# Kernel optimization log

Measured on AMD Instinct MI355X. Metric: run time of the kernel, lower is better.

Reference implementation:

```python
import jax, jax.numpy as jnp
import numpy as np

B, N_TOK, D = 32, 1024, 1024
CH, PS, NP = 3, 16, 32  # channels, patch_size, n_patches (sample_size // patch_size)
EPS = 1e-5


def setup_inputs() -> dict:
    key = jax.random.key(0)
    k1, k2 = jax.random.split(key)
    x = jax.random.normal(k1, (B, N_TOK, D), dtype=jnp.float32)
    ln_w = jnp.ones((D,), dtype=jnp.float32)
    ln_b = jnp.zeros((D,), dtype=jnp.float32)
    W = jax.random.normal(k2, (CH * PS * PS, D), dtype=jnp.float32) * (1.0 / np.sqrt(D))
    b = jnp.zeros((CH * PS * PS,), dtype=jnp.float32)
    return {"x": x, "ln_w": ln_w, "ln_b": ln_b, "W": W, "b": b}


def reference(x, ln_w, ln_b, W, b):
    # LayerNorm over last dim
    mean = jnp.mean(x, axis=-1, keepdims=True)
    var = jnp.mean(jnp.square(x - mean), axis=-1, keepdims=True)
    h = (x - mean) * jax.lax.rsqrt(var + EPS) * ln_w + ln_b
    # SiLU
    h = h * jax.nn.sigmoid(h)
    # Linear: [B, N, D] @ [D, ph*pw*c] + bias
    y = jnp.einsum('bnd,od->bno', h, W) + b  # [B, N_TOK, PS*PS*CH]
    # rearrange 'b (h w) (ph pw c) -> b c (h ph) (w pw)'
    y = y.reshape(B, NP, NP, PS, PS, CH)           # b h w ph pw c
    y = y.transpose(0, 5, 1, 3, 2, 4)              # b c h ph w pw
    y = y.reshape(B, CH, NP * PS, NP * PS)
    return y
```

## Files before the change

kernel.cpp:

```cpp
#include <hip/hip_runtime.h>
#include <hip/hip_bf16.h>

#define M_TOT 32768
#define DDIM  1024
#define ODIM  768
#define LN_EPS 1e-5f

typedef __attribute__((__ext_vector_type__(8))) short bf16x8;
typedef __attribute__((__ext_vector_type__(4))) float f32x4;

__device__ __forceinline__ unsigned short f2bf(float f) {
  union { __hip_bfloat16 h; unsigned short u; } cv;
  cv.h = __float2bfloat16(f);
  return cv.u;
}

__device__ __forceinline__ float silu_f(float v) {
  return v / (1.f + __expf(-v));
}

__global__ void wconv_kernel(const float4* __restrict__ Wf, ushort4* __restrict__ Wb, int n4) {
  int i = blockIdx.x * blockDim.x + threadIdx.x;
  if (i >= n4) return;
  float4 v = Wf[i];
  ushort4 o;
  o.x = f2bf(v.x); o.y = f2bf(v.y); o.z = f2bf(v.z); o.w = f2bf(v.w);
  Wb[i] = o;
}

__global__ __launch_bounds__(256)
void ln_silu_kernel(const float* __restrict__ x, const float* __restrict__ lnw,
                    const float* __restrict__ lnb, __hip_bfloat16* __restrict__ h)
{
  const int tid  = threadIdx.x;
  const int lane = tid & 63;
  const int wid  = tid >> 6;
  const int row  = blockIdx.x * 4 + wid;

  const float4* xr = (const float4*)(x + (size_t)row * DDIM);
  float4 v[4];
#pragma unroll
  for (int jj = 0; jj < 4; ++jj) v[jj] = xr[lane + 64 * jj];

  float s = 0.f, ss = 0.f;
#pragma unroll
  for (int jj = 0; jj < 4; ++jj) {
    float4 a = v[jj];
    s  += a.x + a.y + a.z + a.w;
    ss += a.x * a.x + a.y * a.y + a.z * a.z + a.w * a.w;
  }
#pragma unroll
  for (int off = 1; off < 64; off <<= 1) {
    s  += __shfl_xor(s, off);
    ss += __shfl_xor(ss, off);
  }
  const float mean = s * (1.f / 1024.f);
  const float rstd = rsqrtf(ss * (1.f / 1024.f) - mean * mean + LN_EPS);

  ushort4* hr = (ushort4*)(h + (size_t)row * DDIM);
#pragma unroll
  for (int jj = 0; jj < 4; ++jj) {
    float4 wv = ((const float4*)lnw)[lane + 64 * jj];
    float4 bv = ((const float4*)lnb)[lane + 64 * jj];
    float4 a  = v[jj];
    float e0 = silu_f((a.x - mean) * rstd * wv.x + bv.x);
    float e1 = silu_f((a.y - mean) * rstd * wv.y + bv.y);
    float e2 = silu_f((a.z - mean) * rstd * wv.z + bv.z);
    float e3 = silu_f((a.w - mean) * rstd * wv.w + bv.w);
    ushort4 o; o.x = f2bf(e0); o.y = f2bf(e1); o.z = f2bf(e2); o.w = f2bf(e3);
    hr[lane + 64 * jj] = o;
  }
}

#define GBM 128
#define GBN 192
#define ABYTES 8192
#define BUFB   20480
#define GLDS   61440

__device__ __forceinline__ void gload16(const void* g, void* l) {
  __builtin_amdgcn_global_load_lds(
      (const __attribute__((address_space(1))) unsigned int*)g,
      (__attribute__((address_space(3))) unsigned int*)l, 16, 0, 0);
}

#define VMW(n) asm volatile("s_waitcnt vmcnt(" #n ")" ::: "memory")

__global__ __launch_bounds__(512, 4)
void gemm_kernel(const __hip_bfloat16* __restrict__ h,
                 const __hip_bfloat16* __restrict__ Wb,
                 const float* __restrict__ bias,
                 float* __restrict__ out)
{
  extern __shared__ char smem[];
  const int tid  = threadIdx.x;
  const int lane = tid & 63;
  const int w    = tid >> 6;

  const int wg = blockIdx.x;
  const int sv = ((wg & 7) << 7) + (wg >> 3);
  const int mt = sv >> 2, nt = sv & 3;
  const int m0 = mt * GBM, n0 = nt * GBN;

  const int aRow = tid >> 2;
  const int aSrc = ((tid & 3) ^ (aRow & 3)) << 3;
  const __hip_bfloat16* aPtr = h + (size_t)(m0 + aRow) * DDIM + aSrc;

  const int bRow0 = tid >> 2;
  const int bSrc0 = ((tid & 3) ^ (bRow0 & 3)) << 3;
  const __hip_bfloat16* bPtr0 = Wb + (size_t)(n0 + bRow0) * DDIM + bSrc0;
  const int s1    = 512 + tid;
  const int bRow1 = s1 >> 2;
  const int bSrc1 = ((s1 & 3) ^ (bRow1 & 3)) << 3;
  const __hip_bfloat16* bPtr1 = Wb + (size_t)(n0 + bRow1) * DDIM + bSrc1;
  const bool doB1 = (tid < 256);

  const int wm = w >> 2, wn = w & 3;
  const int lr = lane & 15, lq = lane >> 4;
  int aRd[4], bRd[3];
#pragma unroll
  for (int i = 0; i < 4; ++i) {
    int row = wm * 64 + i * 16 + lr;
    aRd[i] = row * 64 + ((lq ^ (row & 3)) << 4);
  }
#pragma unroll
  for (int j = 0; j < 3; ++j) {
    int row = wn * 48 + j * 16 + lr;
    bRd[j] = ABYTES + row * 64 + ((lq ^ (row & 3)) << 4);
  }

  auto stage = [&](int t) {
    const int k0  = t << 5;
    char* base = smem + (t % 3) * BUFB;
    gload16(aPtr + k0, base + (tid << 4));
    gload16(bPtr0 + k0, base + ABYTES + (tid << 4));
    if (doB1) gload16(bPtr1 + k0, base + ABYTES + (s1 << 4));
  };

  f32x4 acc[4][3];
#pragma unroll
  for (int i = 0; i < 4; ++i)
#pragma unroll
    for (int j = 0; j < 3; ++j)
      acc[i][j] = (f32x4){0.f, 0.f, 0.f, 0.f};

  stage(0); stage(1); stage(2);

  for (int t = 0; t < 32; ++t) {
    if (t <= 29)      { if (w < 4) VMW(6); else VMW(4); }
    else if (t == 30) { if (w < 4) VMW(3); else VMW(2); }
    else              { VMW(0); }
    __builtin_amdgcn_s_barrier();
    asm volatile("" ::: "memory");

    const char* bb = smem + (t % 3) * BUFB;
    bf16x8 af[4], bfq[3];
#pragma unroll
    for (int i = 0; i < 4; ++i) af[i] = *(const bf16x8*)(bb + aRd[i]);
#pragma unroll
    for (int j = 0; j < 3; ++j) bfq[j] = *(const bf16x8*)(bb + bRd[j]);

    __builtin_amdgcn_s_setprio(1);
#pragma unroll
    for (int i = 0; i < 4; ++i)
#pragma unroll
      for (int j = 0; j < 3; ++j)
        acc[i][j] = __builtin_amdgcn_mfma_f32_16x16x32_bf16(af[i], bfq[j], acc[i][j], 0, 0, 0);
    __builtin_amdgcn_s_setprio(0);

    asm volatile("s_waitcnt lgkmcnt(0)" ::: "memory");
    __builtin_amdgcn_s_barrier();
    asm volatile("" ::: "memory");
    if (t <= 28) stage(t + 3);
  }

  const int b   = m0 >> 10;
  const int hq0 = (m0 & 1023) >> 5;
  float bv[3]; int cj[3], pwj[3], prj[3];
#pragma unroll
  for (int j = 0; j < 3; ++j) {
    int o = wn * 48 + j * 16 + lr;
    bv[j]  = bias[n0 + o];
    cj[j]  = o % 3;
    int oq = o / 3;
    pwj[j] = oq & 15;
    prj[j] = o / 48;
  }
  float* ldsF = (float*)smem;

#pragma unroll
  for (int g = 0; g < 8; ++g) {
    if (wm == (g >> 2)) {
      const int i_f = g & 3;
#pragma unroll
      for (int j = 0; j < 3; ++j)
#pragma unroll
        for (int r = 0; r < 4; ++r) {
          const int tk = lq * 4 + r;
          ldsF[((cj[j] * 4 + prj[j]) << 8) + (tk << 4) + (pwj[j] ^ (lq << 2))] =
              acc[i_f][j][r] + bv[j];
        }
    }
    __syncthreads();
    const int hq = hq0 + (g >> 1);
#pragma unroll
    for (int q = 0; q < 2; ++q) {
      if (q == 1 && tid >= 256) break;
      const int f   = (q << 9) + tid;
      const int c   = f >> 8;
      const int pr  = (f >> 6) & 3;
      const int tk  = (f >> 2) & 15;
      const int pw0 = (f & 3) << 2;
      const int lqw = tk >> 2;
      float4 v = *(const float4*)(ldsF + (((c * 4 + pr) << 8) + (tk << 4) + (pw0 ^ (lqw << 2))));
      const size_t idx = (((size_t)(b * 3 + c)) << 18)
                       + (size_t)((hq << 4) + (nt << 2) + pr) * 512
                       + ((g & 1) << 8) + (tk << 4) + pw0;
      *(float4*)(out + idx) = v;
    }
    __syncthreads();
  }
}

#define BM 64
#define BK 32
#define NTHR 1024
#define LDS_BYTES 53760

__global__ __launch_bounds__(NTHR, 4)
void fused_kernel(const float* __restrict__ x,
                  const float* __restrict__ lnw,
                  const float* __restrict__ lnb,
                  const float* __restrict__ Wf,
                  const float* __restrict__ bias,
                  float* __restrict__ out)
{
  extern __shared__ char smem[];
  char* AsBase = smem;
  char* BsBase = smem + 4096;
  float* smean = (float*)(smem + 53248);
  float* srstd = smean + BM;

  const int tid = threadIdx.x;
  const int m0  = blockIdx.x * BM;
  const int bb   = m0 >> 10;
  const int h0   = (m0 & 1023) >> 5;

  {
    const int row = tid >> 4;
    const int sub = tid & 15;
    const float4* xr = (const float4*)(x + (size_t)(m0 + row) * DDIM);
    float s = 0.f, ss = 0.f;
#pragma unroll 4
    for (int j = 0; j < 16; ++j) {
      float4 v = xr[sub + (j << 4)];
      s  += v.x + v.y + v.z + v.w;
      ss += v.x * v.x + v.y * v.y + v.z * v.z + v.w * v.w;
    }
#pragma unroll
    for (int off = 1; off < 16; off <<= 1) {
      s  += __shfl_xor(s, off);
      ss += __shfl_xor(ss, off);
    }
    if (sub == 0) {
      float mean = s * (1.f / 1024.f);
      float var  = ss * (1.f / 1024.f) - mean * mean;
      smean[row] = mean;
      srstd[row] = rsqrtf(var + LN_EPS);
    }
  }
  __syncthreads();

  const int arow  = tid >> 4;
  const int acol2 = tid & 15;
  const int aOff  = (m0 + arow) * DDIM + (acol2 << 1);
  const int aDst  = (arow << 6) + ((((acol2 >> 2) ^ ((arow >> 2) & 3)) << 4)) + ((acol2 & 3) << 2);
  const float aMean = smean[arow];
  const float aRstd = srstd[arow];

  int bOffF[6], bDstF[6];
#pragma unroll
  for (int c = 0; c < 6; ++c) {
    int idx = tid + (c << 10);
    int r = idx >> 3, c4 = idx & 7;
    bOffF[c] = r * DDIM + (c4 << 2);
    bDstF[c] = (r << 6) + ((((c4 >> 1) ^ ((r >> 2) & 3)) << 4)) + ((c4 & 1) << 3);
  }

  const int lane = tid & 63;
  const int wid  = tid >> 6;
  const int lr   = lane & 15;
  const int lq   = lane >> 4;
  const int kswz = (lq ^ ((lr >> 2) & 3)) << 4;
  int aRd[4], bRd[3];
#pragma unroll
  for (int i = 0; i < 4; ++i) aRd[i] = (((i << 4) + lr) << 6) + kswz;
#pragma unroll
  for (int j = 0; j < 3; ++j) bRd[j] = ((wid * 48 + (j << 4) + lr) << 6) + kswz;

  float2 aReg, lwReg, lbReg;
  float4 bRegF[6];

  auto loadTile = [&](int tt) {
    const int k0 = tt * BK;
    aReg  = *(const float2*)(x + aOff + k0);
    lwReg = *(const float2*)(lnw + (acol2 << 1) + k0);
    lbReg = *(const float2*)(lnb + (acol2 << 1) + k0);
#pragma unroll
    for (int c = 0; c < 6; ++c)
      bRegF[c] = *(const float4*)(Wf + bOffF[c] + k0);
  };

  auto storeTile = [&]() {
    float hx = (aReg.x - aMean) * aRstd * lwReg.x + lbReg.x;
    float hy = (aReg.y - aMean) * aRstd * lwReg.y + lbReg.y;
    hx = silu_f(hx); hy = silu_f(hy);
    ushort2 ap; ap.x = f2bf(hx); ap.y = f2bf(hy);
    *(ushort2*)(AsBase + aDst) = ap;
#pragma unroll
    for (int c = 0; c < 6; ++c) {
      float4 wv = bRegF[c];
      ushort4 bp; bp.x = f2bf(wv.x); bp.y = f2bf(wv.y); bp.z = f2bf(wv.z); bp.w = f2bf(wv.w);
      *(ushort4*)(BsBase + bDstF[c]) = bp;
    }
  };

  f32x4 acc[4][3];
#pragma unroll
  for (int i = 0; i < 4; ++i)
#pragma unroll
    for (int j = 0; j < 3; ++j)
      acc[i][j] = (f32x4){0.f, 0.f, 0.f, 0.f};

  loadTile(0);
  storeTile();
  __syncthreads();

  for (int t = 0; t < 32; ++t) {
    if (t < 31) loadTile(t + 1);
    bf16x8 af[4], bfr[3];
#pragma unroll
    for (int i = 0; i < 4; ++i) af[i] = *(const bf16x8*)(AsBase + aRd[i]);
#pragma unroll
    for (int j = 0; j < 3; ++j) bfr[j] = *(const bf16x8*)(BsBase + bRd[j]);
#pragma unroll
    for (int i = 0; i < 4; ++i)
#pragma unroll
      for (int j = 0; j < 3; ++j)
        acc[i][j] = __builtin_amdgcn_mfma_f32_16x16x32_bf16(af[i], bfr[j], acc[i][j], 0, 0, 0);
    __syncthreads();
    if (t < 31) storeTile();
    __syncthreads();
  }

  float* ldsF = (float*)smem;
  float bv[3]; int cv[3], phv[3], pwv[3];
#pragma unroll
  for (int j = 0; j < 3; ++j) {
    const int o = wid * 48 + (j << 4) + lr;
    bv[j]  = bias[o];
    cv[j]  = o % 3;
    const int oq = o / 3;
    pwv[j] = oq & 15;
    phv[j] = oq >> 4;
  }

#pragma unroll
  for (int i = 0; i < 4; ++i) {
#pragma unroll
    for (int j = 0; j < 3; ++j) {
#pragma unroll
      for (int r = 0; r < 4; ++r) {
        const int wl  = (lq << 2) + r;
        const int lin = ((cv[j] * 16 + phv[j]) << 8) + (wl << 4) + pwv[j];
        const int dws = lin ^ (cv[j] << 2) ^ (((lin >> 6) & 1) << 4);
        ldsF[dws] = acc[i][j][r] + bv[j];
      }
    }
    __syncthreads();
    const int hq = h0 + (i >> 1);
    const int w0 = (i & 1) << 4;
#pragma unroll
    for (int q = 0; q < 3; ++q) {
      const int g4  = (q << 10) + tid;
      const int dw  = g4 << 2;
      const int run = dw >> 8;
      const int c   = run >> 4;
      const int ph  = run & 15;
      const int wl  = (dw >> 4) & 15;
      const int pw  = dw & 15;
      const int dws = dw ^ (c << 2) ^ (((dw >> 6) & 1) << 4);
      float4 v = *(const float4*)(ldsF + dws);
      const size_t idx = (((size_t)(bb * 3 + c)) << 18)
                       + ((size_t)((hq << 4) + ph) << 9)
                       + ((w0 + wl) << 4) + pw;
      *(float4*)(out + idx) = v;
    }
    __syncthreads();
  }
}

extern "C" void kernel_launch(void* const* d_in, const int* in_sizes, int n_in,
                              void* d_out, int out_size, void* d_ws, size_t ws_size,
                              hipStream_t stream) {
  const float* x    = (const float*)d_in[0];
  const float* lnw  = (const float*)d_in[1];
  const float* lnb  = (const float*)d_in[2];
  const float* W    = (const float*)d_in[3];
  const float* bias = (const float*)d_in[4];
  float* out = (float*)d_out;

  const size_t wbBytes = (size_t)ODIM * DDIM * sizeof(__hip_bfloat16);
  const size_t hBytes  = (size_t)M_TOT * DDIM * sizeof(__hip_bfloat16);
  __hip_bfloat16* Wb = (__hip_bfloat16*)d_ws;
  __hip_bfloat16* hb = (__hip_bfloat16*)((char*)d_ws + wbBytes);

  if (ws_size >= wbBytes + hBytes) {
    wconv_kernel<<<dim3(768), dim3(256), 0, stream>>>((const float4*)W, (ushort4*)Wb,
                                                      ODIM * DDIM / 4);
    ln_silu_kernel<<<dim3(M_TOT / 4), dim3(256), 0, stream>>>(x, lnw, lnb, hb);
    gemm_kernel<<<dim3((M_TOT / GBM) * (ODIM / GBN)), dim3(512), GLDS, stream>>>(hb, Wb, bias, out);
  } else {
    fused_kernel<<<dim3(M_TOT / BM), dim3(NTHR), LDS_BYTES, stream>>>(
        x, lnw, lnb, W, bias, out);
  }
}
```

Before: 109.7 us.

## Enlarge GEMM tile to 256x192 with split-phase staging and per-warp 64x96 subtiles

The GEMM block tile doubles in M (128 to 256), so each warp now computes a 64x96 subtile with 24 accumulators. Global-to-LDS loads are split into two half-stages issued around the two MFMA halves, with prefetch depth reduced from 3 stages to 2 in a 3-buffer ring. The epilogue LDS layout gains an extra XOR swizzle on the channel parity to reduce bank conflicts. This improves operand reuse per LDS read and halves the number of blocks, at the cost of higher register pressure, occupancy dropping to 2 blocks per CU, and a shallower prefetch pipeline.

```diff
diff --git a/kernel.cpp b/kernel.cpp
--- a/kernel.cpp
+++ b/kernel.cpp
@@ -72,11 +72,11 @@
   }
 }
 
-#define GBM 128
+#define GBM 256
 #define GBN 192
-#define ABYTES 8192
-#define BUFB   20480
-#define GLDS   61440
+#define ABY 16384
+#define BUFB 28672
+#define VMW(n) asm volatile("s_waitcnt vmcnt(" #n ")" ::: "memory")
 
 __device__ __forceinline__ void gload16(const void* g, void* l) {
   __builtin_amdgcn_global_load_lds(
@@ -84,102 +84,111 @@
       (__attribute__((address_space(3))) unsigned int*)l, 16, 0, 0);
 }
 
-#define VMW(n) asm volatile("s_waitcnt vmcnt(" #n ")" ::: "memory")
-
-__global__ __launch_bounds__(512, 4)
+__global__ __launch_bounds__(512, 2)
 void gemm_kernel(const __hip_bfloat16* __restrict__ h,
                  const __hip_bfloat16* __restrict__ Wb,
                  const float* __restrict__ bias,
                  float* __restrict__ out)
 {
-  extern __shared__ char smem[];
+  __shared__ char smem[3 * BUFB];
   const int tid  = threadIdx.x;
   const int lane = tid & 63;
   const int w    = tid >> 6;
 
   const int wg = blockIdx.x;
-  const int sv = ((wg & 7) << 7) + (wg >> 3);
+  const int sv = ((wg & 7) << 6) + (wg >> 3);
   const int mt = sv >> 2, nt = sv & 3;
-  const int m0 = mt * GBM, n0 = nt * GBN;
-
-  const int aRow = tid >> 2;
-  const int aSrc = ((tid & 3) ^ (aRow & 3)) << 3;
-  const __hip_bfloat16* aPtr = h + (size_t)(m0 + aRow) * DDIM + aSrc;
-
-  const int bRow0 = tid >> 2;
-  const int bSrc0 = ((tid & 3) ^ (bRow0 & 3)) << 3;
-  const __hip_bfloat16* bPtr0 = Wb + (size_t)(n0 + bRow0) * DDIM + bSrc0;
-  const int s1    = 512 + tid;
-  const int bRow1 = s1 >> 2;
-  const int bSrc1 = ((s1 & 3) ^ (bRow1 & 3)) << 3;
-  const __hip_bfloat16* bPtr1 = Wb + (size_t)(n0 + bRow1) * DDIM + bSrc1;
-  const bool doB1 = (tid < 256);
-
-  const int wm = w >> 2, wn = w & 3;
+  const int m0 = mt << 8, n0 = nt * GBN;
+
+  const int aR0 = tid >> 2;
+  const __hip_bfloat16* aP0 = h + (size_t)(m0 + aR0) * DDIM + (((tid & 3) ^ (aR0 & 3)) << 3);
+  const int s1  = 512 + tid;
+  const int aR1 = s1 >> 2;
+  const __hip_bfloat16* aP1 = h + (size_t)(m0 + aR1) * DDIM + (((s1 & 3) ^ (aR1 & 3)) << 3);
+  const int bR0 = tid >> 2;
+  const __hip_bfloat16* bP0 = Wb + (size_t)(n0 + bR0) * DDIM + (((tid & 3) ^ (bR0 & 3)) << 3);
+  const int bR1 = s1 >> 2;
+  const __hip_bfloat16* bP1 = Wb + (size_t)(n0 + bR1) * DDIM + (((s1 & 3) ^ (bR1 & 3)) << 3);
+  const bool half = (tid < 256);
+
+  const int wm = w >> 1, wn = w & 1;
   const int lr = lane & 15, lq = lane >> 4;
-  int aRd[4], bRd[3];
+  int aRd[4], bRd[6];
 #pragma unroll
   for (int i = 0; i < 4; ++i) {
     int row = wm * 64 + i * 16 + lr;
     aRd[i] = row * 64 + ((lq ^ (row & 3)) << 4);
   }
 #pragma unroll
-  for (int j = 0; j < 3; ++j) {
-    int row = wn * 48 + j * 16 + lr;
-    bRd[j] = ABYTES + row * 64 + ((lq ^ (row & 3)) << 4);
-  }
-
-  auto stage = [&](int t) {
-    const int k0  = t << 5;
-    char* base = smem + (t % 3) * BUFB;
-    gload16(aPtr + k0, base + (tid << 4));
-    gload16(bPtr0 + k0, base + ABYTES + (tid << 4));
-    if (doB1) gload16(bPtr1 + k0, base + ABYTES + (s1 << 4));
+  for (int j = 0; j < 6; ++j) {
+    int row = wn * 96 + j * 16 + lr;
+    bRd[j] = ABY + row * 64 + ((lq ^ (row & 3)) << 4);
+  }
+
+  auto stP0 = [&](int t) {
+    const int k0 = t << 5;
+    char* b = smem + (t % 3) * BUFB;
+    gload16(aP0 + k0, b + (tid << 4));
+    gload16(bP0 + k0, b + ABY + (tid << 4));
   };
-
-  f32x4 acc[4][3];
+  auto stP1 = [&](int t) {
+    const int k0 = t << 5;
+    char* b = smem + (t % 3) * BUFB;
+    gload16(aP1 + k0, b + (s1 << 4));
+    if (half) gload16(bP1 + k0, b + ABY + (s1 << 4));
+  };
+
+  f32x4 acc[4][6];
 #pragma unroll
   for (int i = 0; i < 4; ++i)
 #pragma unroll
-    for (int j = 0; j < 3; ++j)
+    for (int j = 0; j < 6; ++j)
       acc[i][j] = (f32x4){0.f, 0.f, 0.f, 0.f};
 
-  stage(0); stage(1); stage(2);
+  stP0(0); stP1(0); stP0(1); stP1(1);
 
   for (int t = 0; t < 32; ++t) {
-    if (t <= 29)      { if (w < 4) VMW(6); else VMW(4); }
-    else if (t == 30) { if (w < 4) VMW(3); else VMW(2); }
-    else              { VMW(0); }
+    if (t < 31) { if (half) VMW(4); else VMW(3); }
+    else        { VMW(0); }
     __builtin_amdgcn_s_barrier();
     asm volatile("" ::: "memory");
 
     const char* bb = smem + (t % 3) * BUFB;
-    bf16x8 af[4], bfq[3];
-#pragma unroll
-    for (int i = 0; i < 4; ++i) af[i] = *(const bf16x8*)(bb + aRd[i]);
-#pragma unroll
-    for (int j = 0; j < 3; ++j) bfq[j] = *(const bf16x8*)(bb + bRd[j]);
-
+    if (t < 30) stP0(t + 2);
+    bf16x8 af[4], bf0[3];
+#pragma unroll
+    for (int i = 0; i < 4; ++i) af[i]  = *(const bf16x8*)(bb + aRd[i]);
+#pragma unroll
+    for (int j = 0; j < 3; ++j) bf0[j] = *(const bf16x8*)(bb + bRd[j]);
     __builtin_amdgcn_s_setprio(1);
 #pragma unroll
     for (int i = 0; i < 4; ++i)
 #pragma unroll
       for (int j = 0; j < 3; ++j)
-        acc[i][j] = __builtin_amdgcn_mfma_f32_16x16x32_bf16(af[i], bfq[j], acc[i][j], 0, 0, 0);
+        acc[i][j] = __builtin_amdgcn_mfma_f32_16x16x32_bf16(af[i], bf0[j], acc[i][j], 0, 0, 0);
     __builtin_amdgcn_s_setprio(0);
-
-    asm volatile("s_waitcnt lgkmcnt(0)" ::: "memory");
+    asm volatile("" ::: "memory");
     __builtin_amdgcn_s_barrier();
     asm volatile("" ::: "memory");
-    if (t <= 28) stage(t + 3);
+    if (t < 30) stP1(t + 2);
+    bf16x8 bf1[3];
+#pragma unroll
+    for (int j = 0; j < 3; ++j) bf1[j] = *(const bf16x8*)(bb + bRd[3 + j]);
+    __builtin_amdgcn_s_setprio(1);
+#pragma unroll
+    for (int i = 0; i < 4; ++i)
+#pragma unroll
+      for (int j = 0; j < 3; ++j)
+        acc[i][3 + j] = __builtin_amdgcn_mfma_f32_16x16x32_bf16(af[i], bf1[j], acc[i][3 + j], 0, 0, 0);
+    __builtin_amdgcn_s_setprio(0);
   }
 
   const int b   = m0 >> 10;
   const int hq0 = (m0 & 1023) >> 5;
-  float bv[3]; int cj[3], pwj[3], prj[3];
-#pragma unroll
-  for (int j = 0; j < 3; ++j) {
-    int o = wn * 48 + j * 16 + lr;
+  float bv[6]; int cj[6], pwj[6], prj[6];
+#pragma unroll
+  for (int j = 0; j < 6; ++j) {
+    int o = wn * 96 + j * 16 + lr;
     bv[j]  = bias[n0 + o];
     cj[j]  = o % 3;
     int oq = o / 3;
@@ -189,20 +198,20 @@
   float* ldsF = (float*)smem;
 
 #pragma unroll
-  for (int g = 0; g < 8; ++g) {
+  for (int g = 0; g < 16; ++g) {
     if (wm == (g >> 2)) {
       const int i_f = g & 3;
 #pragma unroll
-      for (int j = 0; j < 3; ++j)
+      for (int j = 0; j < 6; ++j)
 #pragma unroll
         for (int r = 0; r < 4; ++r) {
           const int tk = lq * 4 + r;
-          ldsF[((cj[j] * 4 + prj[j]) << 8) + (tk << 4) + (pwj[j] ^ (lq << 2))] =
+          ldsF[((cj[j] * 4 + prj[j]) << 8) + ((tk ^ (cj[j] & 1)) << 4) + (pwj[j] ^ (lq << 2))] =
               acc[i_f][j][r] + bv[j];
         }
     }
     __syncthreads();
-    const int hq = hq0 + (g >> 1);
+    const int hh = hq0 + (g >> 1);
 #pragma unroll
     for (int q = 0; q < 2; ++q) {
       if (q == 1 && tid >= 256) break;
@@ -212,9 +221,10 @@
       const int tk  = (f >> 2) & 15;
       const int pw0 = (f & 3) << 2;
       const int lqw = tk >> 2;
-      float4 v = *(const float4*)(ldsF + (((c * 4 + pr) << 8) + (tk << 4) + (pw0 ^ (lqw << 2))));
+      float4 v = *(const float4*)(ldsF + (((c * 4 + pr) << 8) + ((tk ^ (c & 1)) << 4)
+                                          + (pw0 ^ (lqw << 2))));
       const size_t idx = (((size_t)(b * 3 + c)) << 18)
-                       + (size_t)((hq << 4) + (nt << 2) + pr) * 512
+                       + (size_t)((hh << 4) + (nt << 2) + pr) * 512
                        + ((g & 1) << 8) + (tk << 4) + pw0;
       *(float4*)(out + idx) = v;
     }
@@ -419,7 +429,7 @@
     wconv_kernel<<<dim3(768), dim3(256), 0, stream>>>((const float4*)W, (ushort4*)Wb,
                                                       ODIM * DDIM / 4);
     ln_silu_kernel<<<dim3(M_TOT / 4), dim3(256), 0, stream>>>(x, lnw, lnb, hb);
-    gemm_kernel<<<dim3((M_TOT / GBM) * (ODIM / GBN)), dim3(512), GLDS, stream>>>(hb, Wb, bias, out);
+    gemm_kernel<<<dim3((M_TOT / GBM) * (ODIM / GBN)), dim3(512), 0, stream>>>(hb, Wb, bias, out);
   } else {
     fused_kernel<<<dim3(M_TOT / BM), dim3(NTHR), LDS_BYTES, stream>>>(
         x, lnw, lnb, W, bias, out);
```

Result: no change. 109.8 us (+0.2%).
